# Kernel optimization log

Measured on AMD Instinct MI355X. Metric: run time of the kernel, lower is better.

Reference implementation:

```python
import jax, jax.numpy as jnp
import numpy as np

EPS = 1e-5       # norm_eps
CHUNK = 64       # scan checkpoint chunk size

def _short_conv(x, w):
    # causal depthwise conv (kernel K) + SiLU; x:[B,T,C], w:[C,K]
    K = w.shape[1]
    T = x.shape[1]
    xp = jnp.pad(x, ((0, 0), (K - 1, 0), (0, 0)))
    y = sum(xp[:, i:i + T, :] * w[:, i] for i in range(K))
    return jax.nn.silu(y)

def _l2norm(x):
    return x * jax.lax.rsqrt(jnp.sum(x * x, -1, keepdims=True) + 1e-6)

def _forward(hidden_states, Wq, Wk, Wv, conv_q, conv_k, conv_v, Wf1, Wf2, Wb,
             A_log, dt_bias, Wg, bg, o_norm_w, Wo):
    B, T, _ = hidden_states.shape
    H = A_log.shape[0]
    x = hidden_states
    q = _short_conv(x @ Wq, conv_q)
    k = _short_conv(x @ Wk, conv_k)
    v = _short_conv(x @ Wv, conv_v)
    Dk = q.shape[-1] // H
    Dv = v.shape[-1] // H
    q = _l2norm(q.reshape(B, T, H, Dk))
    k = _l2norm(k.reshape(B, T, H, Dk))
    v = v.reshape(B, T, H, Dv)
    beta = jax.nn.sigmoid(x @ Wb)                               # [B,T,H]
    g = ((x @ Wf1) @ Wf2).reshape(B, T, H, Dk)
    # KDA gate: g = -exp(A_log) * softplus(g + dt_bias), per head & key channel
    g = -jnp.exp(A_log)[:, None] * jax.nn.softplus(g + dt_bias.reshape(H, Dk))
    gexp = jnp.exp(g)                                           # decay in (0,1)
    scale = Dk ** -0.5

    def step(S, inp):
        q_t, k_t, v_t, ge_t, b_t = inp                          # [B,H,Dk]..., [B,H]
        S = S * ge_t[..., None]                                 # per-key-channel decay
        kv = jnp.einsum('bhk,bhkv->bhv', k_t, S)                # current prediction
        upd = (v_t - kv) * b_t[..., None]                       # delta-rule update
        S = S + jnp.einsum('bhk,bhv->bhkv', k_t, upd)
        o_t = jnp.einsum('bhk,bhkv->bhv', q_t, S) * scale
        return S, o_t

    @jax.checkpoint
    def chunk_fn(S, chunk):
        return jax.lax.scan(step, S, chunk)

    def tm(a):  # [B,T,...] -> [T//CHUNK, CHUNK, B, ...]
        a = jnp.moveaxis(a, 1, 0)
        return a.reshape((T // CHUNK, CHUNK) + a.shape[1:])

    S0 = jnp.zeros((B, H, Dk, Dv), dtype=q.dtype)
    _, o = jax.lax.scan(chunk_fn, S0, (tm(q), tm(k), tm(v), tm(gexp), tm(beta)))
    o = jnp.moveaxis(o.reshape((T, B, H, Dv)), 0, 1)            # [B,T,H,Dv]

    gate_o = (x @ Wg + bg).reshape(B, T, H, Dv)
    on = o * jax.lax.rsqrt(jnp.mean(o * o, -1, keepdims=True) + EPS) * o_norm_w
    on = on * jax.nn.silu(gate_o)                               # gated RMSNorm
    return on.reshape(B, T, H * Dv) @ Wo


def setup_inputs() -> dict:
    key = jax.random.key(0)
    ks = jax.random.split(key, 16)
    B, T, D = 2, 2048, 2048
    H, Dk, Dv, K = 16, 128, 128, 4
    n = jax.random.normal
    return {
        'hidden_states': n(ks[0], (B, T, D), jnp.float32),
        'Wq': n(ks[1], (D, H * Dk), jnp.float32) * D ** -0.5,
        'Wk': n(ks[2], (D, H * Dk), jnp.float32) * D ** -0.5,
        'Wv': n(ks[3], (D, H * Dv), jnp.float32) * D ** -0.5,
        'conv_q': n(ks[4], (H * Dk, K), jnp.float32) * 0.5,
        'conv_k': n(ks[5], (H * Dk, K), jnp.float32) * 0.5,
        'conv_v': n(ks[6], (H * Dv, K), jnp.float32) * 0.5,
        'Wf1': n(ks[7], (D, Dv), jnp.float32) * D ** -0.5,
        'Wf2': n(ks[8], (Dv, H * Dk), jnp.float32) * Dv ** -0.5,
        'Wb': n(ks[9], (D, H), jnp.float32) * D ** -0.5,
        'A_log': jnp.log(jax.random.uniform(ks[10], (H,), jnp.float32, 1.0, 16.0)),
        'dt_bias': jnp.zeros((H * Dk,), jnp.float32),
        'Wg': n(ks[11], (D, H * Dv), jnp.float32) * D ** -0.5,
        'bg': jnp.zeros((H * Dv,), jnp.float32),
        'o_norm_w': jnp.ones((Dv,), jnp.float32),
        'Wo': n(ks[12], (H * Dv, D), jnp.float32) * (H * Dv) ** -0.5,
    }


def reference(hidden_states, Wq, Wk, Wv, conv_q, conv_k, conv_v, Wf1, Wf2, Wb,
              A_log, dt_bias, Wg, bg, o_norm_w, Wo):
    return _forward(hidden_states, Wq, Wk, Wv, conv_q, conv_k, conv_v, Wf1, Wf2,
                    Wb, A_log, dt_bias, Wg, bg, o_norm_w, Wo)
```

## Files before the change

### kernel.cpp

```cpp
#include <hip/hip_runtime.h>
#include <stdint.h>

#define BB 2
#define TT 2048
#define DD 2048
#define HH 16
#define HD 2048
#define MM 4096
#define SCH 16

typedef float f32x4 __attribute__((ext_vector_type(4)));
typedef __bf16 bf16x8 __attribute__((ext_vector_type(8)));
typedef unsigned short u16x4 __attribute__((ext_vector_type(4)));

__device__ __forceinline__ unsigned short f2b(float f) {
  unsigned int u = __float_as_uint(f);
  u += 0x7FFFu + ((u >> 16) & 1u);
  return (unsigned short)(u >> 16);
}

__device__ __forceinline__ void async_ld16(const void* g, void* l) {
  typedef __attribute__((address_space(3))) void as3_t;
  typedef const __attribute__((address_space(1))) void as1_t;
  __builtin_amdgcn_global_load_lds((as1_t*)(uintptr_t)g,
                                   (as3_t*)(unsigned int)(uintptr_t)l, 16, 0, 0);
}

template <int CTRL>
__device__ __forceinline__ float dpp_add(float x) {
  int y = __builtin_amdgcn_update_dpp(0, __float_as_int(x), CTRL, 0xF, 0xF, false);
  return x + __int_as_float(y);
}
__device__ __forceinline__ float reduce16(float x) {
  x = dpp_add<0xB1>(x);
  x = dpp_add<0x4E>(x);
  x = dpp_add<0x124>(x);
  x = dpp_add<0x128>(x);
  return x;
}

__global__ __launch_bounds__(256) void cast_f32_bf16(const float* __restrict__ in,
                                                     unsigned short* __restrict__ out,
                                                     int n4) {
  int i = blockIdx.x * 256 + threadIdx.x;
  if (i >= n4) return;
  f32x4 v = *(const f32x4*)(in + (size_t)i * 4);
  u16x4 r;
  #pragma unroll
  for (int j = 0; j < 4; j++) r[j] = f2b(v[j]);
  *(u16x4*)(out + (size_t)i * 4) = r;
}

__global__ __launch_bounds__(256) void transpose_cast(const float* __restrict__ in,
                                                      unsigned short* __restrict__ out,
                                                      int R, int C) {
  __shared__ float tile[32][33];
  int bx = blockIdx.x * 32, by = blockIdx.y * 32;
  int tx = threadIdx.x, ty = threadIdx.y;
  #pragma unroll
  for (int i = 0; i < 32; i += 8)
    tile[ty + i][tx] = in[(size_t)(by + ty + i) * C + bx + tx];
  __syncthreads();
  #pragma unroll
  for (int i = 0; i < 32; i += 8)
    out[(size_t)(bx + ty + i) * R + by + tx] = f2b(tile[tx][ty + i]);
}

__global__ __launch_bounds__(256) void gemm_bf16(const unsigned short* __restrict__ A,
                                                 const unsigned short* __restrict__ Bt,
                                                 float* __restrict__ C,
                                                 const float* __restrict__ bias,
                                                 int M, int N, int K) {
  __shared__ __align__(16) unsigned short As[128 * 32];
  __shared__ __align__(16) unsigned short Bs[128 * 32];
  int tid = threadIdx.x;
  int l = tid & 63, w = tid >> 6;
  int row0 = blockIdx.y * 128, col0 = blockIdx.x * 128;
  int wm = (w >> 1) * 64, wn = (w & 1) * 64;
  const f32x4 fz = {0.f, 0.f, 0.f, 0.f};
  f32x4 acc[4][4];
  #pragma unroll
  for (int i = 0; i < 4; i++)
    #pragma unroll
    for (int j = 0; j < 4; j++) acc[i][j] = fz;

  int srow = l >> 2, skoff = (l & 3) * 8;
  int quad = l >> 4, mrow = l & 15;

  for (int kt = 0; kt < K; kt += 32) {
    #pragma unroll
    for (int i = 0; i < 2; i++) {
      int c = w * 2 + i;
      const unsigned short* gA = A + (size_t)(row0 + c * 16 + srow) * K + kt + skoff;
      const unsigned short* gB = Bt + (size_t)(col0 + c * 16 + srow) * K + kt + skoff;
      async_ld16(gA, As + c * 512);
      async_ld16(gB, Bs + c * 512);
    }
    __syncthreads();
    bf16x8 af[4], bfr[4];
    #pragma unroll
    for (int i = 0; i < 4; i++)
      af[i] = *(const bf16x8*)(As + (wm + i * 16 + mrow) * 32 + quad * 8);
    #pragma unroll
    for (int j = 0; j < 4; j++)
      bfr[j] = *(const bf16x8*)(Bs + (wn + j * 16 + mrow) * 32 + quad * 8);
    #pragma unroll
    for (int i = 0; i < 4; i++)
      #pragma unroll
      for (int j = 0; j < 4; j++)
        acc[i][j] = __builtin_amdgcn_mfma_f32_16x16x32_bf16(af[i], bfr[j], acc[i][j], 0, 0, 0);
    __syncthreads();
  }
  #pragma unroll
  for (int i = 0; i < 4; i++) {
    #pragma unroll
    for (int j = 0; j < 4; j++) {
      #pragma unroll
      for (int r = 0; r < 4; r++) {
        int rr = row0 + wm + i * 16 + quad * 4 + r;
        int cc = col0 + wn + j * 16 + mrow;
        float v = acc[i][j][r];
        if (bias) v += bias[cc];
        C[(size_t)rr * N + cc] = v;
      }
    }
  }
}

__global__ __launch_bounds__(256) void conv_silu_kernel(const float* __restrict__ Pre,
                                                        const float* __restrict__ cw,
                                                        float* __restrict__ outp,
                                                        int do_norm, float post_mul) {
  int bt = blockIdx.x;
  int b = bt >> 11, t = bt & (TT - 1);
  int tid = threadIdx.x;
  int ch0 = tid * 8;
  f32x4 wv[8];
  #pragma unroll
  for (int j = 0; j < 8; j++) wv[j] = *(const f32x4*)(cw + (size_t)(ch0 + j) * 4);
  float acc[8] = {0, 0, 0, 0, 0, 0, 0, 0};
  #pragma unroll
  for (int i = 0; i < 4; i++) {
    int tt = t - 3 + i;
    if (tt < 0) continue;
    const float* r = Pre + ((size_t)(b * TT + tt)) * HD + ch0;
    f32x4 a0 = *(const f32x4*)r;
    f32x4 a1 = *(const f32x4*)(r + 4);
    #pragma unroll
    for (int j = 0; j < 4; j++) {
      acc[j]     += a0[j] * wv[j][i];
      acc[4 + j] += a1[j] * wv[4 + j][i];
    }
  }
  float val[8];
  #pragma unroll
  for (int j = 0; j < 8; j++) val[j] = acc[j] / (1.f + expf(-acc[j]));
  if (do_norm) {
    float ss = 0.f;
    #pragma unroll
    for (int j = 0; j < 8; j++) ss += val[j] * val[j];
    ss = reduce16(ss);
    float rs = rsqrtf(ss + 1e-6f) * post_mul;
    #pragma unroll
    for (int j = 0; j < 8; j++) val[j] *= rs;
  }
  int h = tid >> 4, cc = (tid & 15) * 8;
  float* op = outp + (((size_t)(b * HH + h)) * TT + t) * 128 + cc;
  f32x4 o0, o1;
  #pragma unroll
  for (int j = 0; j < 4; j++) { o0[j] = val[j]; o1[j] = val[4 + j]; }
  *(f32x4*)op = o0;
  *(f32x4*)(op + 4) = o1;
}

__global__ __launch_bounds__(256) void beta_kernel(const float* __restrict__ x,
                                                   const float* __restrict__ Wb,
                                                   float* __restrict__ beta) {
  __shared__ float xs[2048];
  int bt = blockIdx.x, tid = threadIdx.x;
  int b = bt >> 11, t = bt & (TT - 1);
  const float* row = x + (size_t)bt * DD;
  #pragma unroll
  for (int i = 0; i < 2; i++)
    *(f32x4*)(xs + tid * 8 + i * 4) = *(const f32x4*)(row + tid * 8 + i * 4);
  __syncthreads();
  int h = tid >> 4, seg = tid & 15;
  float p = 0.f;
  for (int j = 0; j < 128; j++) {
    int d = seg * 128 + ((j + seg * 9) & 127);
    p += xs[d] * Wb[(size_t)d * HH + h];
  }
  p = reduce16(p);
  if (seg == 0) beta[((size_t)(b * HH + h)) * TT + t] = 1.f / (1.f + expf(-p));
}

__global__ __launch_bounds__(256) void gexp_kernel(const float* __restrict__ g,
                                                   const float* __restrict__ A_log,
                                                   const float* __restrict__ dt_bias,
                                                   float* __restrict__ ge, int n) {
  int i = blockIdx.x * 256 + threadIdx.x;
  if (i >= n) return;
  int bt = i >> 11, ch = i & (HD - 1);
  int b = bt >> 11, t = bt & (TT - 1);
  int h = ch >> 7, c = ch & 127;
  float gv = g[i] + dt_bias[ch];
  float sp = (gv > 20.f) ? gv : log1pf(expf(gv));
  ge[(((size_t)(b * HH + h)) * TT + t) * 128 + c] = expf(-expf(A_log[h]) * sp);
}

__global__ __launch_bounds__(256) void scan_kernel(const float* __restrict__ q,
                                                   const float* __restrict__ k,
                                                   const float* v,
                                                   const float* __restrict__ ge,
                                                   const float* __restrict__ beta,
                                                   float* o) {
  __shared__ __align__(16) float kbuf[2][SCH * 128];
  __shared__ __align__(16) float gbuf[2][SCH * 128];
  __shared__ __align__(16) float qbuf[2][SCH * 128];
  __shared__ __align__(16) float vbuf[2][SCH * 16];
  __shared__ __align__(16) float bbuf[TT];

  int blk = blockIdx.x;
  int bh = blk & 31;
  int colblk = blk >> 5;
  int tid = threadIdx.x;
  int w = tid >> 6, l = tid & 63;
  int grp = l >> 4, i = l & 15;
  int lcol = w * 4 + grp;
  int col = colblk * 16 + lcol;

  int par = grp & 1;
  int of0 = (2 * i + par) * 4;
  int of1 = (2 * i + (1 - par)) * 4;

  const float* kbh = k    + (size_t)bh * TT * 128;
  const float* gbh = ge   + (size_t)bh * TT * 128;
  const float* qbh = q    + (size_t)bh * TT * 128;
  const float* vbh = v    + (size_t)bh * TT * 128;
  const float* bbh = beta + (size_t)bh * TT;
  float* obh = o + (size_t)bh * TT * 128;

  #pragma unroll
  for (int j = 0; j < 2; j++) {
    int jj = w * 2 + j;
    async_ld16(bbh + jj * 256 + l * 4, (float*)bbuf + jj * 256);
  }
  auto stage = [&](int cidx, int nb) {
    size_t t0 = (size_t)cidx * SCH;
    if (w == 0) {
      #pragma unroll
      for (int j = 0; j < 8; j++)
        async_ld16(kbh + t0 * 128 + j * 256 + l * 4, (float*)kbuf[nb] + j * 256);
    } else if (w == 1) {
      #pragma unroll
      for (int j = 0; j < 8; j++)
        async_ld16(gbh + t0 * 128 + j * 256 + l * 4, (float*)gbuf[nb] + j * 256);
    } else if (w == 2) {
      #pragma unroll
      for (int j = 0; j < 8; j++)
        async_ld16(qbh + t0 * 128 + j * 256 + l * 4, (float*)qbuf[nb] + j * 256);
    } else {
      async_ld16(vbh + (t0 + (size_t)(l >> 2)) * 128 + colblk * 16 + (l & 3) * 4,
                 (float*)vbuf[nb]);
    }
  };
  stage(0, 0);
  __syncthreads();

  f32x4 s0 = {0.f, 0.f, 0.f, 0.f}, s1 = {0.f, 0.f, 0.f, 0.f};
  float okeep = 0.f;

  for (int c = 0; c < TT / SCH; c++) {
    int cb = c & 1, nb = cb ^ 1;
    if (c + 1 < TT / SCH) stage(c + 1, nb);

    const float* kc = (const float*)kbuf[cb];
    const float* gc = (const float*)gbuf[cb];
    const float* qc = (const float*)qbuf[cb];
    float vbt[SCH], btp[SCH];
    #pragma unroll
    for (int s = 0; s < SCH; s++) {
      float vv = ((const float*)vbuf[cb])[s * 16 + lcol];
      float bb = bbuf[c * SCH + s];
      btp[s] = bb;
      vbt[s] = vv * bb;
    }
    f32x4 k0 = *(const f32x4*)(kc + of0), k1 = *(const f32x4*)(kc + of1);
    f32x4 g0 = *(const f32x4*)(gc + of0), g1 = *(const f32x4*)(gc + of1);
    f32x4 q0 = *(const f32x4*)(qc + of0), q1 = *(const f32x4*)(qc + of1);
    #pragma unroll
    for (int s = 0; s < SCH; s++) {
      f32x4 k0n, k1n, g0n, g1n, q0n, q1n;
      if (s + 1 < SCH) {
        const float* kp = kc + (s + 1) * 128;
        const float* gp = gc + (s + 1) * 128;
        const float* qp = qc + (s + 1) * 128;
        k0n = *(const f32x4*)(kp + of0); k1n = *(const f32x4*)(kp + of1);
        g0n = *(const f32x4*)(gp + of0); g1n = *(const f32x4*)(gp + of1);
        q0n = *(const f32x4*)(qp + of0); q1n = *(const f32x4*)(qp + of1);
      }
      f32x4 kg0 = k0 * g0, kg1 = k1 * g1;
      f32x4 pp = kg0 * s0 + kg1 * s1;
      float p = (pp[0] + pp[1]) + (pp[2] + pp[3]);
      p = reduce16(p);
      s0 *= g0; s1 *= g1;
      float u = fmaf(-btp[s], p, vbt[s]);
      s0 += k0 * u; s1 += k1 * u;
      f32x4 oo = q0 * s0 + q1 * s1;
      float po = (oo[0] + oo[1]) + (oo[2] + oo[3]);
      po = reduce16(po);
      okeep = (i == s) ? po : okeep;
      if (s + 1 < SCH) {
        k0 = k0n; k1 = k1n; g0 = g0n; g1 = g1n; q0 = q0n; q1 = q1n;
      }
    }
    obh[((size_t)c * SCH + i) * 128 + col] = okeep;
    __syncthreads();
  }
}

__global__ __launch_bounds__(256) void out_norm_kernel(const float* o,
                                                       const float* __restrict__ gate,
                                                       const float* __restrict__ w,
                                                       unsigned short* __restrict__ onb) {
  int bt = blockIdx.x, tid = threadIdx.x;
  int b = bt >> 11, t = bt & (TT - 1);
  int h = tid >> 4, seg = tid & 15;
  size_t obase = (((size_t)(b * HH + h)) * TT + t) * 128 + seg * 8;
  size_t gbase = (size_t)bt * HD + (size_t)h * 128 + seg * 8;
  f32x4 o0 = *(const f32x4*)(o + obase);
  f32x4 o1 = *(const f32x4*)(o + obase + 4);
  float ss = 0.f;
  #pragma unroll
  for (int j = 0; j < 4; j++) ss += o0[j] * o0[j] + o1[j] * o1[j];
  ss = reduce16(ss);
  float rs = rsqrtf(ss * (1.f / 128.f) + 1e-5f);
  u16x4 r0, r1;
  #pragma unroll
  for (int j = 0; j < 4; j++) {
    float gv0 = gate[gbase + j];
    float gv1 = gate[gbase + 4 + j];
    float a0 = o0[j] * rs * w[seg * 8 + j] * (gv0 / (1.f + expf(-gv0)));
    float a1 = o1[j] * rs * w[seg * 8 + 4 + j] * (gv1 / (1.f + expf(-gv1)));
    r0[j] = f2b(a0);
    r1[j] = f2b(a1);
  }
  *(u16x4*)(onb + gbase) = r0;
  *(u16x4*)(onb + gbase + 4) = r1;
}

extern "C" void kernel_launch(void* const* d_in, const int* in_sizes, int n_in,
                              void* d_out, int out_size, void* d_ws, size_t ws_size,
                              hipStream_t stream) {
  const float* x       = (const float*)d_in[0];
  const float* Wq      = (const float*)d_in[1];
  const float* Wk      = (const float*)d_in[2];
  const float* Wv      = (const float*)d_in[3];
  const float* cq      = (const float*)d_in[4];
  const float* ck      = (const float*)d_in[5];
  const float* cv      = (const float*)d_in[6];
  const float* Wf1     = (const float*)d_in[7];
  const float* Wf2     = (const float*)d_in[8];
  const float* Wb      = (const float*)d_in[9];
  const float* A_log   = (const float*)d_in[10];
  const float* dt_bias = (const float*)d_in[11];
  const float* Wg      = (const float*)d_in[12];
  const float* bg      = (const float*)d_in[13];
  const float* onw     = (const float*)d_in[14];
  const float* Wo      = (const float*)d_in[15];
  float* out = (float*)d_out;

  char* ws = (char*)d_ws;
  unsigned short* WT  = (unsigned short*)(ws);
  unsigned short* xb  = (unsigned short*)(ws + ((size_t)8  << 20));
  float* P    = (float*)(ws + ((size_t)24  << 20));
  float* qb   = (float*)(ws + ((size_t)56  << 20));
  float* kb   = (float*)(ws + ((size_t)88  << 20));
  float* vb   = (float*)(ws + ((size_t)120 << 20));
  float* geb  = (float*)(ws + ((size_t)152 << 20));
  float* betab= (float*)(ws + ((size_t)184 << 20));
  float* f1   = (float*)(ws + ((size_t)185 << 20));
  unsigned short* f1b = (unsigned short*)(ws + ((size_t)187 << 20));
  unsigned short* onb = xb;
  float* gateb = P;
  float* ob    = vb;

  dim3 tb(32, 8);
  dim3 gemm_grid(HD / 128, MM / 128);

  cast_f32_bf16<<<(MM * DD / 4 + 255) / 256, 256, 0, stream>>>(x, xb, MM * DD / 4);

  transpose_cast<<<dim3(HD / 32, DD / 32), tb, 0, stream>>>(Wq, WT, DD, HD);
  gemm_bf16<<<gemm_grid, 256, 0, stream>>>(xb, WT, P, nullptr, MM, HD, DD);
  conv_silu_kernel<<<MM, 256, 0, stream>>>(P, cq, qb, 1, 0.08838834764831845f);
  transpose_cast<<<dim3(HD / 32, DD / 32), tb, 0, stream>>>(Wk, WT, DD, HD);
  gemm_bf16<<<gemm_grid, 256, 0, stream>>>(xb, WT, P, nullptr, MM, HD, DD);
  conv_silu_kernel<<<MM, 256, 0, stream>>>(P, ck, kb, 1, 1.0f);
  transpose_cast<<<dim3(HD / 32, DD / 32), tb, 0, stream>>>(Wv, WT, DD, HD);
  gemm_bf16<<<gemm_grid, 256, 0, stream>>>(xb, WT, P, nullptr, MM, HD, DD);
  conv_silu_kernel<<<MM, 256, 0, stream>>>(P, cv, vb, 0, 1.0f);

  beta_kernel<<<MM, 256, 0, stream>>>(x, Wb, betab);

  transpose_cast<<<dim3(128 / 32, DD / 32), tb, 0, stream>>>(Wf1, WT, DD, 128);
  gemm_bf16<<<dim3(1, MM / 128), 256, 0, stream>>>(xb, WT, f1, nullptr, MM, 128, DD);
  cast_f32_bf16<<<(MM * 128 / 4 + 255) / 256, 256, 0, stream>>>(f1, f1b, MM * 128 / 4);
  transpose_cast<<<dim3(HD / 32, 128 / 32), tb, 0, stream>>>(Wf2, WT, 128, HD);
  gemm_bf16<<<gemm_grid, 256, 0, stream>>>(f1b, WT, P, nullptr, MM, HD, 128);
  gexp_kernel<<<(MM * HD + 255) / 256, 256, 0, stream>>>(P, A_log, dt_bias, geb, MM * HD);

  transpose_cast<<<dim3(HD / 32, DD / 32), tb, 0, stream>>>(Wg, WT, DD, HD);
  gemm_bf16<<<gemm_grid, 256, 0, stream>>>(xb, WT, gateb, bg, MM, HD, DD);

  scan_kernel<<<BB * HH * 8, 256, 0, stream>>>(qb, kb, vb, geb, betab, ob);

  out_norm_kernel<<<MM, 256, 0, stream>>>(ob, gateb, onw, onb);

  transpose_cast<<<dim3(DD / 32, HD / 32), tb, 0, stream>>>(Wo, WT, HD, DD);
  gemm_bf16<<<dim3(DD / 128, MM / 128), 256, 0, stream>>>(onb, WT, out, nullptr, MM, DD, HD);
}
```

Before: 1.208 ms.

## Remap GEMM block order, deepen scan LDS prefetch, add scan occupancy bound

The GEMM kernel now maps block IDs through a strided permutation over groups of eight when the block count allows. The likely aim is to spread neighbouring tiles across chiplets or XCDs for better L2 locality. The scan kernel's inner loop now prefetches LDS operands two timesteps ahead instead of one, to hide more LDS latency behind the serial recurrence. It also declares launch_bounds(256,1), giving the compiler more register room. The deeper prefetch raises register pressure, and the block remap may change cache behaviour either way.

```diff
diff --git a/kernel.cpp b/kernel.cpp
--- a/kernel.cpp
+++ b/kernel.cpp
@@ -75,7 +75,17 @@
   __shared__ __align__(16) unsigned short Bs[128 * 32];
   int tid = threadIdx.x;
   int l = tid & 63, w = tid >> 6;
-  int row0 = blockIdx.y * 128, col0 = blockIdx.x * 128;
+
+  int nbx = gridDim.x;
+  int tot = nbx * gridDim.y;
+  int id = blockIdx.y * nbx + blockIdx.x;
+  int nid = id;
+  if ((tot & 7) == 0) {
+    int per = tot >> 3;
+    nid = (id & 7) * per + (id >> 3);
+  }
+  int row0 = (nid / nbx) * 128, col0 = (nid % nbx) * 128;
+
   int wm = (w >> 1) * 64, wn = (w & 1) * 64;
   const f32x4 fz = {0.f, 0.f, 0.f, 0.f};
   f32x4 acc[4][4];
@@ -208,12 +218,12 @@
   ge[(((size_t)(b * HH + h)) * TT + t) * 128 + c] = expf(-expf(A_log[h]) * sp);
 }
 
-__global__ __launch_bounds__(256) void scan_kernel(const float* __restrict__ q,
-                                                   const float* __restrict__ k,
-                                                   const float* v,
-                                                   const float* __restrict__ ge,
-                                                   const float* __restrict__ beta,
-                                                   float* o) {
+__global__ __launch_bounds__(256, 1) void scan_kernel(const float* __restrict__ q,
+                                                      const float* __restrict__ k,
+                                                      const float* v,
+                                                      const float* __restrict__ ge,
+                                                      const float* __restrict__ beta,
+                                                      float* o) {
   __shared__ __align__(16) float kbuf[2][SCH * 128];
   __shared__ __align__(16) float gbuf[2][SCH * 128];
   __shared__ __align__(16) float qbuf[2][SCH * 128];
@@ -285,33 +295,39 @@
       btp[s] = bb;
       vbt[s] = vv * bb;
     }
-    f32x4 k0 = *(const f32x4*)(kc + of0), k1 = *(const f32x4*)(kc + of1);
-    f32x4 g0 = *(const f32x4*)(gc + of0), g1 = *(const f32x4*)(gc + of1);
-    f32x4 q0 = *(const f32x4*)(qc + of0), q1 = *(const f32x4*)(qc + of1);
+    f32x4 ka0 = *(const f32x4*)(kc + of0), ka1 = *(const f32x4*)(kc + of1);
+    f32x4 ga0 = *(const f32x4*)(gc + of0), ga1 = *(const f32x4*)(gc + of1);
+    f32x4 qa0 = *(const f32x4*)(qc + of0), qa1 = *(const f32x4*)(qc + of1);
+    f32x4 kb0 = *(const f32x4*)(kc + 128 + of0), kb1 = *(const f32x4*)(kc + 128 + of1);
+    f32x4 gb0 = *(const f32x4*)(gc + 128 + of0), gb1 = *(const f32x4*)(gc + 128 + of1);
+    f32x4 qb0 = *(const f32x4*)(qc + 128 + of0), qb1 = *(const f32x4*)(qc + 128 + of1);
     #pragma unroll
     for (int s = 0; s < SCH; s++) {
-      f32x4 k0n, k1n, g0n, g1n, q0n, q1n;
-      if (s + 1 < SCH) {
-        const float* kp = kc + (s + 1) * 128;
-        const float* gp = gc + (s + 1) * 128;
-        const float* qp = qc + (s + 1) * 128;
-        k0n = *(const f32x4*)(kp + of0); k1n = *(const f32x4*)(kp + of1);
-        g0n = *(const f32x4*)(gp + of0); g1n = *(const f32x4*)(gp + of1);
-        q0n = *(const f32x4*)(qp + of0); q1n = *(const f32x4*)(qp + of1);
+      f32x4 kf0, kf1, gf0, gf1, qf0, qf1;
+      if (s + 2 < SCH) {
+        const float* kp = kc + (s + 2) * 128;
+        const float* gp = gc + (s + 2) * 128;
+        const float* qp = qc + (s + 2) * 128;
+        kf0 = *(const f32x4*)(kp + of0); kf1 = *(const f32x4*)(kp + of1);
+        gf0 = *(const f32x4*)(gp + of0); gf1 = *(const f32x4*)(gp + of1);
+        qf0 = *(const f32x4*)(qp + of0); qf1 = *(const f32x4*)(qp + of1);
       }
-      f32x4 kg0 = k0 * g0, kg1 = k1 * g1;
+      f32x4 kg0 = ka0 * ga0, kg1 = ka1 * ga1;
       f32x4 pp = kg0 * s0 + kg1 * s1;
       float p = (pp[0] + pp[1]) + (pp[2] + pp[3]);
       p = reduce16(p);
-      s0 *= g0; s1 *= g1;
+      s0 *= ga0; s1 *= ga1;
       float u = fmaf(-btp[s], p, vbt[s]);
-      s0 += k0 * u; s1 += k1 * u;
-      f32x4 oo = q0 * s0 + q1 * s1;
+      s0 += ka0 * u; s1 += ka1 * u;
+      f32x4 oo = qa0 * s0 + qa1 * s1;
       float po = (oo[0] + oo[1]) + (oo[2] + oo[3]);
       po = reduce16(po);
       okeep = (i == s) ? po : okeep;
       if (s + 1 < SCH) {
-        k0 = k0n; k1 = k1n; g0 = g0n; g1 = g1n; q0 = q0n; q1 = q1n;
+        ka0 = kb0; ka1 = kb1; ga0 = gb0; ga1 = gb1; qa0 = qb0; qa1 = qb1;
+        if (s + 2 < SCH) {
+          kb0 = kf0; kb1 = kf1; gb0 = gf0; gb1 = gf1; qb0 = qf0; qb1 = qf1;
+        }
       }
     }
     obh[((size_t)c * SCH + i) * 128 + col] = okeep;
```

Result: no change. 1.184 ms (-1.9%).

## Fuse QKV projections into one GEMM with bf16 head-major outputs

Applied to the files above, without the earlier changes.

Concatenates the transposed Wq/Wk/Wv weights and runs one wide GEMM whose epilogue writes bf16 results directly in head-major layout, so the conv kernels read half the bytes. The gate GEMM also outputs bf16, GEMM blocks are remapped with an 8-way grouped tile ordering, and the scan kernel gets an occupancy hint. This cuts launch count and intermediate memory traffic, at the cost of extra bf16 rounding of pre-conv activations and the gate, plus scattered 2-byte epilogue stores.

```diff
diff --git a/kernel.cpp b/kernel.cpp
--- a/kernel.cpp
+++ b/kernel.cpp
@@ -12,6 +12,7 @@
 typedef float f32x4 __attribute__((ext_vector_type(4)));
 typedef __bf16 bf16x8 __attribute__((ext_vector_type(8)));
 typedef unsigned short u16x4 __attribute__((ext_vector_type(4)));
+typedef unsigned int u32x4 __attribute__((ext_vector_type(4)));
 
 __device__ __forceinline__ unsigned short f2b(float f) {
   unsigned int u = __float_as_uint(f);
@@ -66,55 +67,55 @@
     out[(size_t)(bx + ty + i) * R + by + tx] = f2b(tile[tx][ty + i]);
 }
 
+#define GEMM_PROLOGUE_AND_LOOP                                                         \
+  __shared__ __align__(16) unsigned short As[128 * 32];                                \
+  __shared__ __align__(16) unsigned short Bs[128 * 32];                                \
+  int tid = threadIdx.x;                                                               \
+  int l = tid & 63, w = tid >> 6;                                                      \
+  int nbx = gridDim.x;                                                                 \
+  int tot = nbx * gridDim.y;                                                           \
+  int id = blockIdx.y * nbx + blockIdx.x;                                              \
+  int nid = id;                                                                        \
+  if ((tot & 7) == 0) { int per = tot >> 3; nid = (id & 7) * per + (id >> 3); }        \
+  int row0 = (nid / nbx) * 128, col0 = (nid % nbx) * 128;                              \
+  int wm = (w >> 1) * 64, wn = (w & 1) * 64;                                           \
+  const f32x4 fz = {0.f, 0.f, 0.f, 0.f};                                               \
+  f32x4 acc[4][4];                                                                     \
+  _Pragma("unroll") for (int i = 0; i < 4; i++)                                        \
+    _Pragma("unroll") for (int j = 0; j < 4; j++) acc[i][j] = fz;                      \
+  int srow = l >> 2, skoff = (l & 3) * 8;                                              \
+  int quad = l >> 4, mrow = l & 15;                                                    \
+  for (int kt = 0; kt < K; kt += 32) {                                                 \
+    _Pragma("unroll") for (int i = 0; i < 2; i++) {                                    \
+      int c = w * 2 + i;                                                               \
+      const unsigned short* gA = A + (size_t)(row0 + c * 16 + srow) * K + kt + skoff;  \
+      const unsigned short* gB = Bt + (size_t)(col0 + c * 16 + srow) * K + kt + skoff; \
+      async_ld16(gA, As + c * 512);                                                    \
+      async_ld16(gB, Bs + c * 512);                                                    \
+    }                                                                                  \
+    __syncthreads();                                                                   \
+    bf16x8 af[4], bfr[4];                                                              \
+    _Pragma("unroll") for (int i = 0; i < 4; i++)                                      \
+      af[i] = *(const bf16x8*)(As + (wm + i * 16 + mrow) * 32 + quad * 8);             \
+    _Pragma("unroll") for (int j = 0; j < 4; j++)                                      \
+      bfr[j] = *(const bf16x8*)(Bs + (wn + j * 16 + mrow) * 32 + quad * 8);            \
+    _Pragma("unroll") for (int i = 0; i < 4; i++)                                      \
+      _Pragma("unroll") for (int j = 0; j < 4; j++)                                    \
+        acc[i][j] = __builtin_amdgcn_mfma_f32_16x16x32_bf16(af[i], bfr[j], acc[i][j],  \
+                                                            0, 0, 0);                  \
+    __syncthreads();                                                                   \
+  }
+
 __global__ __launch_bounds__(256) void gemm_bf16(const unsigned short* __restrict__ A,
                                                  const unsigned short* __restrict__ Bt,
                                                  float* __restrict__ C,
                                                  const float* __restrict__ bias,
                                                  int M, int N, int K) {
-  __shared__ __align__(16) unsigned short As[128 * 32];
-  __shared__ __align__(16) unsigned short Bs[128 * 32];
-  int tid = threadIdx.x;
-  int l = tid & 63, w = tid >> 6;
-  int row0 = blockIdx.y * 128, col0 = blockIdx.x * 128;
-  int wm = (w >> 1) * 64, wn = (w & 1) * 64;
-  const f32x4 fz = {0.f, 0.f, 0.f, 0.f};
-  f32x4 acc[4][4];
+  GEMM_PROLOGUE_AND_LOOP
   #pragma unroll
   for (int i = 0; i < 4; i++)
     #pragma unroll
-    for (int j = 0; j < 4; j++) acc[i][j] = fz;
-
-  int srow = l >> 2, skoff = (l & 3) * 8;
-  int quad = l >> 4, mrow = l & 15;
-
-  for (int kt = 0; kt < K; kt += 32) {
-    #pragma unroll
-    for (int i = 0; i < 2; i++) {
-      int c = w * 2 + i;
-      const unsigned short* gA = A + (size_t)(row0 + c * 16 + srow) * K + kt + skoff;
-      const unsigned short* gB = Bt + (size_t)(col0 + c * 16 + srow) * K + kt + skoff;
-      async_ld16(gA, As + c * 512);
-      async_ld16(gB, Bs + c * 512);
-    }
-    __syncthreads();
-    bf16x8 af[4], bfr[4];
-    #pragma unroll
-    for (int i = 0; i < 4; i++)
-      af[i] = *(const bf16x8*)(As + (wm + i * 16 + mrow) * 32 + quad * 8);
-    #pragma unroll
     for (int j = 0; j < 4; j++)
-      bfr[j] = *(const bf16x8*)(Bs + (wn + j * 16 + mrow) * 32 + quad * 8);
-    #pragma unroll
-    for (int i = 0; i < 4; i++)
-      #pragma unroll
-      for (int j = 0; j < 4; j++)
-        acc[i][j] = __builtin_amdgcn_mfma_f32_16x16x32_bf16(af[i], bfr[j], acc[i][j], 0, 0, 0);
-    __syncthreads();
-  }
-  #pragma unroll
-  for (int i = 0; i < 4; i++) {
-    #pragma unroll
-    for (int j = 0; j < 4; j++) {
       #pragma unroll
       for (int r = 0; r < 4; r++) {
         int rr = row0 + wm + i * 16 + quad * 4 + r;
@@ -123,11 +124,55 @@
         if (bias) v += bias[cc];
         C[(size_t)rr * N + cc] = v;
       }
-    }
-  }
-}
-
-__global__ __launch_bounds__(256) void conv_silu_kernel(const float* __restrict__ Pre,
+}
+
+__global__ __launch_bounds__(256) void gemm_bf16_bout(const unsigned short* __restrict__ A,
+                                                      const unsigned short* __restrict__ Bt,
+                                                      unsigned short* __restrict__ C,
+                                                      const float* __restrict__ bias,
+                                                      int M, int N, int K) {
+  GEMM_PROLOGUE_AND_LOOP
+  #pragma unroll
+  for (int i = 0; i < 4; i++)
+    #pragma unroll
+    for (int j = 0; j < 4; j++)
+      #pragma unroll
+      for (int r = 0; r < 4; r++) {
+        int rr = row0 + wm + i * 16 + quad * 4 + r;
+        int cc = col0 + wn + j * 16 + mrow;
+        C[(size_t)rr * N + cc] = f2b(acc[i][j][r] + bias[cc]);
+      }
+}
+
+__global__ __launch_bounds__(256) void gemm_qkv(const unsigned short* __restrict__ A,
+                                                const unsigned short* __restrict__ Bt,
+                                                unsigned short* __restrict__ Dq,
+                                                unsigned short* __restrict__ Dk,
+                                                unsigned short* __restrict__ Dv,
+                                                int M, int N, int K) {
+  GEMM_PROLOGUE_AND_LOOP
+  {
+    int cc0 = col0 + wn + mrow;
+    (void)cc0;
+  }
+  #pragma unroll
+  for (int i = 0; i < 4; i++)
+    #pragma unroll
+    for (int j = 0; j < 4; j++)
+      #pragma unroll
+      for (int r = 0; r < 4; r++) {
+        int rr = row0 + wm + i * 16 + quad * 4 + r;
+        int cc = col0 + wn + j * 16 + mrow;
+        int sub = cc >> 11;
+        int ch = cc & (HD - 1);
+        int h = ch >> 7, c2 = ch & 127;
+        int b = rr >> 11, t = rr & (TT - 1);
+        unsigned short* dst = (sub == 0) ? Dq : (sub == 1) ? Dk : Dv;
+        dst[(((size_t)(b * HH + h)) * TT + t) * 128 + c2] = f2b(acc[i][j][r]);
+      }
+}
+
+__global__ __launch_bounds__(256) void conv_silu_kernel(const unsigned short* __restrict__ Pre,
                                                         const float* __restrict__ cw,
                                                         float* __restrict__ outp,
                                                         int do_norm, float post_mul) {
@@ -135,22 +180,25 @@
   int b = bt >> 11, t = bt & (TT - 1);
   int tid = threadIdx.x;
   int ch0 = tid * 8;
+  int h = tid >> 4, c0 = (tid & 15) * 8;
   f32x4 wv[8];
   #pragma unroll
   for (int j = 0; j < 8; j++) wv[j] = *(const f32x4*)(cw + (size_t)(ch0 + j) * 4);
   float acc[8] = {0, 0, 0, 0, 0, 0, 0, 0};
+  const unsigned short* base = Pre + (((size_t)(b * HH + h)) * TT) * 128 + c0;
   #pragma unroll
   for (int i = 0; i < 4; i++) {
     int tt = t - 3 + i;
     if (tt < 0) continue;
-    const float* r = Pre + ((size_t)(b * TT + tt)) * HD + ch0;
-    f32x4 a0 = *(const f32x4*)r;
-    f32x4 a1 = *(const f32x4*)(r + 4);
-    #pragma unroll
-    for (int j = 0; j < 4; j++) {
-      acc[j]     += a0[j] * wv[j][i];
-      acc[4 + j] += a1[j] * wv[4 + j][i];
+    u32x4 raw = *(const u32x4*)(base + (size_t)tt * 128);
+    float e[8];
+    #pragma unroll
+    for (int jj = 0; jj < 4; jj++) {
+      e[2 * jj]     = __uint_as_float(raw[jj] << 16);
+      e[2 * jj + 1] = __uint_as_float(raw[jj] & 0xffff0000u);
     }
+    #pragma unroll
+    for (int j = 0; j < 8; j++) acc[j] += e[j] * wv[j][i];
   }
   float val[8];
   #pragma unroll
@@ -164,8 +212,7 @@
     #pragma unroll
     for (int j = 0; j < 8; j++) val[j] *= rs;
   }
-  int h = tid >> 4, cc = (tid & 15) * 8;
-  float* op = outp + (((size_t)(b * HH + h)) * TT + t) * 128 + cc;
+  float* op = outp + (((size_t)(b * HH + h)) * TT + t) * 128 + c0;
   f32x4 o0, o1;
   #pragma unroll
   for (int j = 0; j < 4; j++) { o0[j] = val[j]; o1[j] = val[4 + j]; }
@@ -208,12 +255,12 @@
   ge[(((size_t)(b * HH + h)) * TT + t) * 128 + c] = expf(-expf(A_log[h]) * sp);
 }
 
-__global__ __launch_bounds__(256) void scan_kernel(const float* __restrict__ q,
-                                                   const float* __restrict__ k,
-                                                   const float* v,
-                                                   const float* __restrict__ ge,
-                                                   const float* __restrict__ beta,
-                                                   float* o) {
+__global__ __launch_bounds__(256, 1) void scan_kernel(const float* __restrict__ q,
+                                                      const float* __restrict__ k,
+                                                      const float* v,
+                                                      const float* __restrict__ ge,
+                                                      const float* __restrict__ beta,
+                                                      float* o) {
   __shared__ __align__(16) float kbuf[2][SCH * 128];
   __shared__ __align__(16) float gbuf[2][SCH * 128];
   __shared__ __align__(16) float qbuf[2][SCH * 128];
@@ -320,7 +367,7 @@
 }
 
 __global__ __launch_bounds__(256) void out_norm_kernel(const float* o,
-                                                       const float* __restrict__ gate,
+                                                       const unsigned short* __restrict__ gate,
                                                        const float* __restrict__ w,
                                                        unsigned short* __restrict__ onb) {
   int bt = blockIdx.x, tid = threadIdx.x;
@@ -330,6 +377,13 @@
   size_t gbase = (size_t)bt * HD + (size_t)h * 128 + seg * 8;
   f32x4 o0 = *(const f32x4*)(o + obase);
   f32x4 o1 = *(const f32x4*)(o + obase + 4);
+  u32x4 graw = *(const u32x4*)(gate + gbase);
+  float gv[8];
+  #pragma unroll
+  for (int jj = 0; jj < 4; jj++) {
+    gv[2 * jj]     = __uint_as_float(graw[jj] << 16);
+    gv[2 * jj + 1] = __uint_as_float(graw[jj] & 0xffff0000u);
+  }
   float ss = 0.f;
   #pragma unroll
   for (int j = 0; j < 4; j++) ss += o0[j] * o0[j] + o1[j] * o1[j];
@@ -338,8 +392,8 @@
   u16x4 r0, r1;
   #pragma unroll
   for (int j = 0; j < 4; j++) {
-    float gv0 = gate[gbase + j];
-    float gv1 = gate[gbase + 4 + j];
+    float gv0 = gv[j];
+    float gv1 = gv[4 + j];
     float a0 = o0[j] * rs * w[seg * 8 + j] * (gv0 / (1.f + expf(-gv0)));
     float a1 = o1[j] * rs * w[seg * 8 + 4 + j] * (gv1 / (1.f + expf(-gv1)));
     r0[j] = f2b(a0);
@@ -372,47 +426,49 @@
 
   char* ws = (char*)d_ws;
   unsigned short* WT  = (unsigned short*)(ws);
-  unsigned short* xb  = (unsigned short*)(ws + ((size_t)8  << 20));
-  float* P    = (float*)(ws + ((size_t)24  << 20));
-  float* qb   = (float*)(ws + ((size_t)56  << 20));
-  float* kb   = (float*)(ws + ((size_t)88  << 20));
-  float* vb   = (float*)(ws + ((size_t)120 << 20));
-  float* geb  = (float*)(ws + ((size_t)152 << 20));
-  float* betab= (float*)(ws + ((size_t)184 << 20));
-  float* f1   = (float*)(ws + ((size_t)185 << 20));
-  unsigned short* f1b = (unsigned short*)(ws + ((size_t)187 << 20));
+  unsigned short* xb  = (unsigned short*)(ws + ((size_t)24 << 20));
+  float* geb          = (float*)(ws + ((size_t)40 << 20));
+  float* P2           = (float*)(ws + ((size_t)72 << 20));
+  unsigned short* B1  = (unsigned short*)(ws + ((size_t)72 << 20));
+  unsigned short* B2  = (unsigned short*)(ws + ((size_t)88 << 20));
+  unsigned short* B3  = (unsigned short*)(ws + ((size_t)104 << 20));
+  float* qc           = (float*)(ws + ((size_t)120 << 20));
+  float* kc           = (float*)(ws + ((size_t)152 << 20));
+  float* vc           = (float*)(ws + ((size_t)72 << 20));
+  unsigned short* gateb = (unsigned short*)(ws + ((size_t)104 << 20));
+  float* f1           = (float*)(ws + ((size_t)184 << 20));
+  unsigned short* f1b = (unsigned short*)(ws + ((size_t)186 << 20));
+  float* betab        = (float*)(ws + ((size_t)187 << 20));
   unsigned short* onb = xb;
-  float* gateb = P;
-  float* ob    = vb;
+  float* ob = vc;
 
   dim3 tb(32, 8);
-  dim3 gemm_grid(HD / 128, MM / 128);
 
   cast_f32_bf16<<<(MM * DD / 4 + 255) / 256, 256, 0, stream>>>(x, xb, MM * DD / 4);
-
-  transpose_cast<<<dim3(HD / 32, DD / 32), tb, 0, stream>>>(Wq, WT, DD, HD);
-  gemm_bf16<<<gemm_grid, 256, 0, stream>>>(xb, WT, P, nullptr, MM, HD, DD);
-  conv_silu_kernel<<<MM, 256, 0, stream>>>(P, cq, qb, 1, 0.08838834764831845f);
-  transpose_cast<<<dim3(HD / 32, DD / 32), tb, 0, stream>>>(Wk, WT, DD, HD);
-  gemm_bf16<<<gemm_grid, 256, 0, stream>>>(xb, WT, P, nullptr, MM, HD, DD);
-  conv_silu_kernel<<<MM, 256, 0, stream>>>(P, ck, kb, 1, 1.0f);
-  transpose_cast<<<dim3(HD / 32, DD / 32), tb, 0, stream>>>(Wv, WT, DD, HD);
-  gemm_bf16<<<gemm_grid, 256, 0, stream>>>(xb, WT, P, nullptr, MM, HD, DD);
-  conv_silu_kernel<<<MM, 256, 0, stream>>>(P, cv, vb, 0, 1.0f);
-
-  beta_kernel<<<MM, 256, 0, stream>>>(x, Wb, betab);
 
   transpose_cast<<<dim3(128 / 32, DD / 32), tb, 0, stream>>>(Wf1, WT, DD, 128);
   gemm_bf16<<<dim3(1, MM / 128), 256, 0, stream>>>(xb, WT, f1, nullptr, MM, 128, DD);
   cast_f32_bf16<<<(MM * 128 / 4 + 255) / 256, 256, 0, stream>>>(f1, f1b, MM * 128 / 4);
   transpose_cast<<<dim3(HD / 32, 128 / 32), tb, 0, stream>>>(Wf2, WT, 128, HD);
-  gemm_bf16<<<gemm_grid, 256, 0, stream>>>(f1b, WT, P, nullptr, MM, HD, 128);
-  gexp_kernel<<<(MM * HD + 255) / 256, 256, 0, stream>>>(P, A_log, dt_bias, geb, MM * HD);
+  gemm_bf16<<<dim3(HD / 128, MM / 128), 256, 0, stream>>>(f1b, WT, P2, nullptr, MM, HD, 128);
+  gexp_kernel<<<(MM * HD + 255) / 256, 256, 0, stream>>>(P2, A_log, dt_bias, geb, MM * HD);
+
+  beta_kernel<<<MM, 256, 0, stream>>>(x, Wb, betab);
+
+  transpose_cast<<<dim3(HD / 32, DD / 32), tb, 0, stream>>>(Wq, WT, DD, HD);
+  transpose_cast<<<dim3(HD / 32, DD / 32), tb, 0, stream>>>(Wk, WT + (size_t)2048 * 2048, DD, HD);
+  transpose_cast<<<dim3(HD / 32, DD / 32), tb, 0, stream>>>(Wv, WT + (size_t)4096 * 2048, DD, HD);
+
+  gemm_qkv<<<dim3(6144 / 128, MM / 128), 256, 0, stream>>>(xb, WT, B1, B2, B3, MM, 6144, DD);
+
+  conv_silu_kernel<<<MM, 256, 0, stream>>>(B1, cq, qc, 1, 0.08838834764831845f);
+  conv_silu_kernel<<<MM, 256, 0, stream>>>(B2, ck, kc, 1, 1.0f);
+  conv_silu_kernel<<<MM, 256, 0, stream>>>(B3, cv, vc, 0, 1.0f);
 
   transpose_cast<<<dim3(HD / 32, DD / 32), tb, 0, stream>>>(Wg, WT, DD, HD);
-  gemm_bf16<<<gemm_grid, 256, 0, stream>>>(xb, WT, gateb, bg, MM, HD, DD);
-
-  scan_kernel<<<BB * HH * 8, 256, 0, stream>>>(qb, kb, vb, geb, betab, ob);
+  gemm_bf16_bout<<<dim3(HD / 128, MM / 128), 256, 0, stream>>>(xb, WT, gateb, bg, MM, HD, DD);
+
+  scan_kernel<<<BB * HH * 8, 256, 0, stream>>>(qc, kc, vc, geb, betab, ob);
 
   out_norm_kernel<<<MM, 256, 0, stream>>>(ob, gateb, onw, onb);
 
```

New measurement: 1.152 ms. 1.05x faster.
